# Kernel optimization log

Measured on AMD Instinct MI355X. Metric: run time of the kernel, lower is better.

## Reference

```python
import jax, jax.numpy as jnp
import numpy as np

N_NODES = 50000


def _gcn_conv(x, src, dst, W, b, n_nodes):
    # x: [N, Fin] -> h: [N, Fout]; GCN: D^-1/2 (A+I) D^-1/2 (x W) + b
    h = x @ W
    deg = jax.ops.segment_sum(jnp.ones_like(dst, dtype=h.dtype), dst,
                              num_segments=n_nodes)
    dinv = jax.lax.rsqrt(jnp.maximum(deg, 1.0))
    norm = dinv[src] * dinv[dst]                      # [E]
    msg = h[src] * norm[:, None]                      # [E, Fout] gather
    agg = jax.ops.segment_sum(msg, dst, num_segments=n_nodes)  # scatter-add
    return agg + b


def setup_inputs() -> dict:
    key = jax.random.key(0)
    k0, k1, k2, k3 = jax.random.split(key, 4)
    N, E, F_IN, H, C = N_NODES, 800000, 128, 128, 16
    x = jax.random.normal(k0, (N, F_IN), dtype=jnp.float32)
    edge_index = jax.random.randint(k1, (2, E), 0, N, dtype=jnp.int64)
    W1 = jax.random.normal(k2, (F_IN, H), dtype=jnp.float32) / np.sqrt(F_IN)
    b1 = jnp.zeros((H,), dtype=jnp.float32)
    W2 = jax.random.normal(k3, (H, C), dtype=jnp.float32) / np.sqrt(H)
    b2 = jnp.zeros((C,), dtype=jnp.float32)
    return {"x": x, "edge_index": edge_index, "W1": W1, "b1": b1,
            "W2": W2, "b2": b2}


def reference(x, edge_index, W1, b1, W2, b2):
    n = x.shape[0]
    # add self-loops (shared by both conv layers)
    loops = jnp.arange(n, dtype=edge_index.dtype)
    src = jnp.concatenate([edge_index[0], loops])
    dst = jnp.concatenate([edge_index[1], loops])
    h = _gcn_conv(x, src, dst, W1, b1, n)
    h = jax.nn.relu(h)
    # dropout p=0.5 is identity in eval mode
    h = _gcn_conv(h, src, dst, W2, b2, n)
    return jax.nn.log_softmax(h, axis=1)
```

## Files before the change

### kernel.cpp

```cpp
#include <hip/hip_runtime.h>
#include <hip/hip_fp16.h>
#include <math.h>


#define NBUCKET_SHIFT 8
#define BIN_CHUNK 4096
#define PAD_SLOP (7 << NBUCKET_SHIFT)
#define CAP  5120
#define CCAP (CAP + PAD_SLOP)

typedef __bf16 bf16x8 __attribute__((ext_vector_type(8)));
typedef float  f32x4  __attribute__((ext_vector_type(4)));
typedef float  f32x2  __attribute__((ext_vector_type(2)));

__device__ __forceinline__ unsigned short pack_bf16(float f) {
    unsigned u = __float_as_uint(f);
    return (unsigned short)((u + 0x7fffu + ((u >> 16) & 1u)) >> 16);
}

__device__ __forceinline__ void acc_fp8x16_fma(f32x2* a, uint4 v, float w) {
    f32x2 ww; ww.x = w; ww.y = w;
    a[0] += __builtin_amdgcn_cvt_pk_f32_fp8(v.x, false) * ww;
    a[1] += __builtin_amdgcn_cvt_pk_f32_fp8(v.x, true)  * ww;
    a[2] += __builtin_amdgcn_cvt_pk_f32_fp8(v.y, false) * ww;
    a[3] += __builtin_amdgcn_cvt_pk_f32_fp8(v.y, true)  * ww;
    a[4] += __builtin_amdgcn_cvt_pk_f32_fp8(v.z, false) * ww;
    a[5] += __builtin_amdgcn_cvt_pk_f32_fp8(v.z, true)  * ww;
    a[6] += __builtin_amdgcn_cvt_pk_f32_fp8(v.w, false) * ww;
    a[7] += __builtin_amdgcn_cvt_pk_f32_fp8(v.w, true)  * ww;
}

__device__ __forceinline__ void acc_fp16x8(f32x2* a, uint4 v) {
    float2 f;
    f = __half22float2(*(const __half2*)&v.x); a[0] += *(f32x2*)&f;
    f = __half22float2(*(const __half2*)&v.y); a[1] += *(f32x2*)&f;
    f = __half22float2(*(const __half2*)&v.z); a[2] += *(f32x2*)&f;
    f = __half22float2(*(const __half2*)&v.w); a[3] += *(f32x2*)&f;
}

union K1Smem {
    struct { unsigned spair[BIN_CHUNK]; int lcnt[256]; int lbase[256]; } b;
    unsigned short wtp[16384];
    float outb[4][16 * 132];
};

__global__ __launch_bounds__(256)
void bin_gemm1_kernel(const int* __restrict__ src, const int* __restrict__ dst,
                      int* __restrict__ bcur, unsigned* __restrict__ pairs,
                      int E, int nbuckets, int nbins,
                      const float* __restrict__ x, const float* __restrict__ W1,
                      unsigned* __restrict__ h1b, int N) {
    __shared__ K1Smem sm;
    const int blk = blockIdx.x;
    const int tid = threadIdx.x;

    if (blk < nbins) {
        const int e0 = blk * BIN_CHUNK;
        const int cnt = min(BIN_CHUNK, E - e0);
        sm.b.lcnt[tid] = 0;
        __syncthreads();
        for (int i = tid; i < cnt; i += 256) {
            unsigned s = (unsigned)src[e0 + i], d = (unsigned)dst[e0 + i];
            sm.b.spair[i] = (d >> NBUCKET_SHIFT) << 24 | (d & 255u) << 16 | s;
            atomicAdd(&sm.b.lcnt[d >> NBUCKET_SHIFT], 1);
        }
        __syncthreads();
        if (tid < nbuckets) {
            int c = sm.b.lcnt[tid];
            sm.b.lbase[tid] = (c > 0) ? atomicAdd(&bcur[tid], c) : 0;
            sm.b.lcnt[tid] = 0;
        }
        __syncthreads();
        for (int i = tid; i < cnt; i += 256) {
            unsigned p = sm.b.spair[i];
            int b = (int)(p >> 24);
            int off = atomicAdd(&sm.b.lcnt[b], 1);
            pairs[b * CAP + sm.b.lbase[b] + off] = p;
        }
        return;
    }

    const int gblk = blk - nbins;
    const int wave = tid >> 6, lane = tid & 63;
    const int q = lane >> 4, m = lane & 15;
    const int row0 = gblk * 64 + wave * 16;
    const int row = row0 + m;
    const int rowc = (row < N) ? row : (N - 1);

    for (int it = tid; it < 16384; it += 256) {
        int k = it >> 7, n = it & 127;
        int t = n >> 4, mm = n & 15;
        int ks = k >> 5;
        int lane2 = (((k & 31) >> 3) << 4) | mm;
        int j = k & 7;
        sm.wtp[(t * 4 + ks) * 512 + lane2 * 8 + j] = pack_bf16(W1[it]);
    }
    __syncthreads();

    f32x4 acc[8];
#pragma unroll
    for (int t = 0; t < 8; t++) acc[t] = (f32x4)0.0f;

#pragma unroll
    for (int ks = 0; ks < 4; ks++) {
        const float4* xp = (const float4*)(x + (size_t)rowc * 128 + ks * 32 + q * 8);
        float4 f0 = xp[0], f1 = xp[1];
        float fv[8] = {f0.x, f0.y, f0.z, f0.w, f1.x, f1.y, f1.z, f1.w};
        bf16x8 ah, al;
#pragma unroll
        for (int j = 0; j < 8; j++) {
            __bf16 h = (__bf16)fv[j];
            ah[j] = h;
            al[j] = (__bf16)(fv[j] - (float)h);
        }
#pragma unroll
        for (int t = 0; t < 8; t++) {
            bf16x8 b = *(const bf16x8*)(sm.wtp + (size_t)(t * 4 + ks) * 512 + lane * 8);
            acc[t] = __builtin_amdgcn_mfma_f32_16x16x32_bf16(ah, b, acc[t], 0, 0, 0);
            acc[t] = __builtin_amdgcn_mfma_f32_16x16x32_bf16(al, b, acc[t], 0, 0, 0);
        }
    }
    __syncthreads();

#pragma unroll
    for (int t = 0; t < 8; t++)
#pragma unroll
        for (int r = 0; r < 4; r++)
            sm.outb[wave][(q * 4 + r) * 132 + t * 16 + m] = acc[t][r];
    __syncthreads();

    const int r2 = lane >> 2, j = lane & 3;
    const int orow = row0 + r2;
    if (orow < N) {
        const float* lrow = &sm.outb[wave][r2 * 132];
#pragma unroll
        for (int s = 0; s < 4; s++) {
            float4 a = *(const float4*)(lrow + s * 32 + j * 8);
            float4 b = *(const float4*)(lrow + s * 32 + j * 8 + 4);
            unsigned lo = __builtin_amdgcn_cvt_pk_fp8_f32(a.x, a.y, 0, false);
            lo = __builtin_amdgcn_cvt_pk_fp8_f32(a.z, a.w, lo, true);
            unsigned hi = __builtin_amdgcn_cvt_pk_fp8_f32(b.x, b.y, 0, false);
            hi = __builtin_amdgcn_cvt_pk_fp8_f32(b.z, b.w, hi, true);
            ((uint2*)h1b)[(size_t)orow * 16 + s * 4 + j] = make_uint2(lo, hi);
        }
    }
}

__global__ __launch_bounds__(256)
void bucket_build_kernel(const int* __restrict__ bcur, const unsigned* __restrict__ pairs,
                         int* __restrict__ rowptr, int* __restrict__ rowcnt,
                         float* __restrict__ dinv, int* __restrict__ colsrc,
                         unsigned* __restrict__ h1b, unsigned* __restrict__ h2u,
                         int N, int nbuckets) {
    __shared__ int cnt[256];
    __shared__ int sm[256];
    const int tid = threadIdx.x;
    const int blk = blockIdx.x;
    const int nb0 = blk << NBUCKET_SHIFT;

    if (blk == 0) {
        if (tid < 32) h1b[(size_t)N * 32 + tid] = 0u;
        else if (tid < 40) h2u[(size_t)N * 8 + (tid - 32)] = 0u;
        else if (tid == 40) dinv[N] = 0.0f;
    }

    const int lo = blk * CAP;
    const int hi = lo + bcur[blk];
    cnt[tid] = 0;
    __syncthreads();

    for (int i = lo + tid; i < hi; i += 256)
        atomicAdd(&cnt[(int)(pairs[i] >> 16) & 255], 1);
    __syncthreads();

    int v = cnt[tid];
    int pdeg = (v + 7) & ~7;
    sm[tid] = pdeg;
    __syncthreads();
#pragma unroll
    for (int off = 1; off < 256; off <<= 1) {
        int u = (tid >= off) ? sm[tid - off] : 0;
        __syncthreads();
        sm[tid] += u;
        __syncthreads();
    }
    int pexcl = sm[tid] - pdeg;
    const int start = blk * CCAP + pexcl;
    int node = nb0 + tid;
    if (node < N) {
        rowptr[node] = start;
        rowcnt[node] = pdeg;
        dinv[node] = rsqrtf((float)v + 1.0f);
    }
    __syncthreads();
    cnt[tid] = start;
    __syncthreads();
    for (int i = lo + tid; i < hi; i += 256) {
        unsigned p = pairs[i];
        int pos = atomicAdd(&cnt[(int)(p >> 16) & 255], 1);
        colsrc[pos] = (int)(p & 0xffffu);
    }
    for (int p = start + v; p < start + pdeg; ++p)
        colsrc[p] = N;
}

__global__ __launch_bounds__(256)
void l1_fused_kernel(const int* __restrict__ rowptr, const int* __restrict__ rowcnt,
                     const int* __restrict__ colsrc,
                     const float* __restrict__ dinv, const unsigned* __restrict__ h1b,
                     const float* __restrict__ b1, const float* __restrict__ W2,
                     __half* __restrict__ h2s, int N) {
    __shared__ float rows[4][2][132];
    __shared__ float w2s[128 * 16];
    const int tid = threadIdx.x;
    const int wave = tid >> 6, lane = tid & 63;
    const int c = lane & 7;
    const int g = (lane >> 3) & 3;
    const int n = lane >> 5;
    const int d = blockIdx.x * 8 + wave * 2 + n;

    for (int i = tid; i < 512; i += 256)
        ((float4*)w2s)[i] = ((const float4*)W2)[i];

    const uint4* hq = (const uint4*)h1b;

    if (d < N) {
        const float dvd = dinv[d];
        f32x2 a[8];
#pragma unroll
        for (int j = 0; j < 8; j++) a[j] = (f32x2)0.0f;

        if (g == 0)
            acc_fp8x16_fma(a, hq[(size_t)d * 8 + c], dvd);

        int i = rowptr[d];
        const int end = i + rowcnt[d];
        int s0 = 0, s1 = 0, s2 = 0, s3 = 0;
        if (i + 16 <= end) {
            s0 = colsrc[i + g];      s1 = colsrc[i + g + 4];
            s2 = colsrc[i + g + 8];  s3 = colsrc[i + g + 12];
        }
        while (i + 16 <= end) {
            uint4 v0 = hq[(size_t)s0 * 8 + c];
            uint4 v1 = hq[(size_t)s1 * 8 + c];
            uint4 v2 = hq[(size_t)s2 * 8 + c];
            uint4 v3 = hq[(size_t)s3 * 8 + c];
            float w0 = dinv[s0], w1 = dinv[s1], w2 = dinv[s2], w3 = dinv[s3];
            i += 16;
            if (i + 16 <= end) {
                s0 = colsrc[i + g];      s1 = colsrc[i + g + 4];
                s2 = colsrc[i + g + 8];  s3 = colsrc[i + g + 12];
            }
            acc_fp8x16_fma(a, v0, w0); acc_fp8x16_fma(a, v1, w1);
            acc_fp8x16_fma(a, v2, w2); acc_fp8x16_fma(a, v3, w3);
        }
        for (; i + 4 <= end; i += 4) {
            int sx = colsrc[i + g];
            acc_fp8x16_fma(a, hq[(size_t)sx * 8 + c], dinv[sx]);
        }

#pragma unroll
        for (int j = 0; j < 8; j++) {
            a[j].x += __shfl_xor(a[j].x, 8, 64);
            a[j].y += __shfl_xor(a[j].y, 8, 64);
            a[j].x += __shfl_xor(a[j].x, 16, 64);
            a[j].y += __shfl_xor(a[j].y, 16, 64);
        }

        if (g == 0) {
            float* rbase = &rows[wave][n][c * 16];
#pragma unroll
            for (int t = 0; t < 4; t++) {
                float4 bb = ((const float4*)b1)[c * 4 + t];
                float4 o;
                o.x = fmaxf(a[2 * t].x * dvd + bb.x, 0.0f);
                o.y = fmaxf(a[2 * t].y * dvd + bb.y, 0.0f);
                o.z = fmaxf(a[2 * t + 1].x * dvd + bb.z, 0.0f);
                o.w = fmaxf(a[2 * t + 1].y * dvd + bb.w, 0.0f);
                *(float4*)(rbase + 4 * t) = o;
            }
        }
    }
    __syncthreads();

    const int n2 = lane >> 5, kh = (lane >> 4) & 1, col = lane & 15;
    const int d2 = blockIdx.x * 8 + wave * 2 + n2;
    if (d2 < N) {
        const float* r = &rows[wave][n2][kh * 64];
        const float* w = &w2s[kh * 64 * 16];
        float p = 0.0f;
#pragma unroll
        for (int k = 0; k < 64; k++)
            p = fmaf(r[k], w[k * 16 + col], p);
        p += __shfl_xor(p, 16, 64);
        if (kh == 0)
            h2s[(size_t)d2 * 16 + col] = __float2half_rn(p * dinv[d2]);
    }
}

__global__ __launch_bounds__(256)
void l2_kernel(const int* __restrict__ rowptr, const int* __restrict__ rowcnt,
               const int* __restrict__ colsrc,
               const float* __restrict__ dinv, const unsigned* __restrict__ h2s,
               const float* __restrict__ b2, float* __restrict__ out, int N) {
    const int tid = threadIdx.x;
    const int wave = tid >> 6, lane = tid & 63;
    const int n = lane >> 4;
    const int g = (lane >> 1) & 7;
    const int c = lane & 1;
    const int d = blockIdx.x * 16 + wave * 4 + n;
    if (d >= N) return;
    const uint4* h2q = (const uint4*)h2s;

    f32x2 a[4];
#pragma unroll
    for (int j = 0; j < 4; j++) a[j] = (f32x2)0.0f;

    if (g == 0)
        acc_fp16x8(a, h2q[(size_t)d * 2 + c]);

    int i = rowptr[d];
    const int end = i + rowcnt[d];
    uint4 v; int s2 = 0;
    if (i < end) {
        int s = colsrc[i + g];
        v = h2q[(size_t)s * 2 + c];
    }
    if (i + 8 < end) s2 = colsrc[i + 8 + g];
    while (i < end) {
        uint4 vc = v;
        if (i + 8 < end) v = h2q[(size_t)s2 * 2 + c];
        if (i + 16 < end) s2 = colsrc[i + 16 + g];
        i += 8;
        acc_fp16x8(a, vc);
    }

#pragma unroll
    for (int j = 0; j < 4; j++) {
#pragma unroll
        for (int off = 2; off <= 8; off <<= 1) {
            a[j].x += __shfl_xor(a[j].x, off, 64);
            a[j].y += __shfl_xor(a[j].y, off, 64);
        }
    }

    const float dv = dinv[d];
    const float* af = (const float*)a;
    float v8[8];
#pragma unroll
    for (int j = 0; j < 8; j++) v8[j] = af[j] * dv + b2[c * 8 + j];

    float m = v8[0];
#pragma unroll
    for (int j = 1; j < 8; j++) m = fmaxf(m, v8[j]);
    m = fmaxf(m, __shfl_xor(m, 1, 64));
    float e = 0.0f;
#pragma unroll
    for (int j = 0; j < 8; j++) e += expf(v8[j] - m);
    e += __shfl_xor(e, 1, 64);
    float lse = m + logf(e);

    if (g == 0) {
        float4 o0 = make_float4(v8[0] - lse, v8[1] - lse, v8[2] - lse, v8[3] - lse);
        float4 o1 = make_float4(v8[4] - lse, v8[5] - lse, v8[6] - lse, v8[7] - lse);
        float4* op = (float4*)(out + (size_t)d * 16 + c * 8);
        op[0] = o0; op[1] = o1;
    }
}

extern "C" void kernel_launch(void* const* d_in, const int* in_sizes, int n_in,
                              void* d_out, int out_size, void* d_ws, size_t ws_size,
                              hipStream_t stream) {
    const float* x  = (const float*)d_in[0];
    const int*  ei  = (const int*)d_in[1];
    const float* W1 = (const float*)d_in[2];
    const float* b1 = (const float*)d_in[3];
    const float* W2 = (const float*)d_in[4];
    const float* b2 = (const float*)d_in[5];
    float* out = (float*)d_out;

    const int N = in_sizes[0] / 128;
    const int E = in_sizes[1] / 2;
    const int* src = ei;
    const int* dst = ei + E;
    const int nbuckets = (N + 255) >> NBUCKET_SHIFT;
    const int nbins = (E + BIN_CHUNK - 1) / BIN_CHUNK;
    const int g1blocks = (N + 63) / 64;

    float*          wsf     = (float*)d_ws;
    float*          dinv    = wsf;
    int*            rowptr  = (int*)(wsf + N + 16);
    int*            rowcnt  = rowptr + N;
    int*            bcur    = rowcnt + N;
    int*            colsrc  = bcur + 256;
    unsigned*       pairs   = (unsigned*)(colsrc + (size_t)nbuckets * CCAP);
    unsigned*       h1b     = pairs + (size_t)nbuckets * CAP;
    unsigned*       h2u     = h1b + (size_t)(N + 1) * 32;

    hipMemsetAsync(bcur, 0, 256 * sizeof(int), stream);
    bin_gemm1_kernel<<<nbins + g1blocks, 256, 0, stream>>>(src, dst, bcur, pairs,
                                                           E, nbuckets, nbins,
                                                           x, W1, h1b, N);

    bucket_build_kernel<<<nbuckets, 256, 0, stream>>>(bcur, pairs, rowptr, rowcnt,
                                                      dinv, colsrc, h1b, h2u,
                                                      N, nbuckets);

    l1_fused_kernel<<<(N + 7) / 8, 256, 0, stream>>>(rowptr, rowcnt, colsrc, dinv,
                                                     h1b, b1, W2, (__half*)h2u, N);

    l2_kernel<<<(N + 15) / 16, 256, 0, stream>>>(rowptr, rowcnt, colsrc, dinv, h2u,
                                                 b2, out, N);
}
```

Baseline: 160.3 us.

## Split layer-1 features into two 64-column halves and accumulate partial GEMM2 atomically

Stores the fp8 hidden features as two separate 64-column planes, so the layer-1 gather kernel processes one half per block and the per-neighbour gather footprint per plane is halved, which should improve cache locality. Each half computes a partial product with its slice of W2 and atomically adds into an fp32 h2 accumulator that is zeroed by an enlarged memset. Layer 2 now gathers fp32 rows and folds the source-side dinv scaling into the gather instead of the stored fp16 pre-scaled values. The cost is twice as many gather passes over colsrc and dinv, extra atomics, a larger memset, and doubled bytes per layer-2 gather.

```diff
diff --git a/kernel.cpp b/kernel.cpp
--- a/kernel.cpp
+++ b/kernel.cpp
@@ -30,14 +30,6 @@
     a[7] += __builtin_amdgcn_cvt_pk_f32_fp8(v.w, true)  * ww;
 }
 
-__device__ __forceinline__ void acc_fp16x8(f32x2* a, uint4 v) {
-    float2 f;
-    f = __half22float2(*(const __half2*)&v.x); a[0] += *(f32x2*)&f;
-    f = __half22float2(*(const __half2*)&v.y); a[1] += *(f32x2*)&f;
-    f = __half22float2(*(const __half2*)&v.z); a[2] += *(f32x2*)&f;
-    f = __half22float2(*(const __half2*)&v.w); a[3] += *(f32x2*)&f;
-}
-
 union K1Smem {
     struct { unsigned spair[BIN_CHUNK]; int lcnt[256]; int lbase[256]; } b;
     unsigned short wtp[16384];
@@ -141,7 +133,8 @@
             lo = __builtin_amdgcn_cvt_pk_fp8_f32(a.z, a.w, lo, true);
             unsigned hi = __builtin_amdgcn_cvt_pk_fp8_f32(b.x, b.y, 0, false);
             hi = __builtin_amdgcn_cvt_pk_fp8_f32(b.z, b.w, hi, true);
-            ((uint2*)h1b)[(size_t)orow * 16 + s * 4 + j] = make_uint2(lo, hi);
+            ((uint2*)h1b)[((size_t)(s >> 1) * (N + 1) + orow) * 8 + (s & 1) * 4 + j]
+                = make_uint2(lo, hi);
         }
     }
 }
@@ -150,8 +143,7 @@
 void bucket_build_kernel(const int* __restrict__ bcur, const unsigned* __restrict__ pairs,
                          int* __restrict__ rowptr, int* __restrict__ rowcnt,
                          float* __restrict__ dinv, int* __restrict__ colsrc,
-                         unsigned* __restrict__ h1b, unsigned* __restrict__ h2u,
-                         int N, int nbuckets) {
+                         unsigned* __restrict__ h1b, int N, int nbuckets) {
     __shared__ int cnt[256];
     __shared__ int sm[256];
     const int tid = threadIdx.x;
@@ -159,9 +151,9 @@
     const int nb0 = blk << NBUCKET_SHIFT;
 
     if (blk == 0) {
-        if (tid < 32) h1b[(size_t)N * 32 + tid] = 0u;
-        else if (tid < 40) h2u[(size_t)N * 8 + (tid - 32)] = 0u;
-        else if (tid == 40) dinv[N] = 0.0f;
+        if (tid < 16) h1b[((size_t)0 * (N + 1) + N) * 16 + tid] = 0u;
+        else if (tid < 32) h1b[((size_t)1 * (N + 1) + N) * 16 + (tid - 16)] = 0u;
+        else if (tid == 32) dinv[N] = 0.0f;
     }
 
     const int lo = blk * CAP;
@@ -209,20 +201,21 @@
                      const int* __restrict__ colsrc,
                      const float* __restrict__ dinv, const unsigned* __restrict__ h1b,
                      const float* __restrict__ b1, const float* __restrict__ W2,
-                     __half* __restrict__ h2s, int N) {
-    __shared__ float rows[4][2][132];
-    __shared__ float w2s[128 * 16];
+                     float* __restrict__ h2acc, int N) {
+    __shared__ float rows[4][4][68];
+    __shared__ float w2s[64 * 16];
     const int tid = threadIdx.x;
     const int wave = tid >> 6, lane = tid & 63;
-    const int c = lane & 7;
-    const int g = (lane >> 3) & 3;
-    const int n = lane >> 5;
-    const int d = blockIdx.x * 8 + wave * 2 + n;
-
-    for (int i = tid; i < 512; i += 256)
-        ((float4*)w2s)[i] = ((const float4*)W2)[i];
-
-    const uint4* hq = (const uint4*)h1b;
+    const int c = lane & 3;
+    const int g = (lane >> 2) & 3;
+    const int n = lane >> 4;
+    const int p = blockIdx.x & 1;
+    const int d = (blockIdx.x >> 1) * 16 + wave * 4 + n;
+
+    for (int i = tid; i < 256; i += 256)
+        ((float4*)w2s)[i] = ((const float4*)W2)[p * 256 + i];
+
+    const uint4* hq = (const uint4*)h1b + (size_t)p * (N + 1) * 4;
 
     if (d < N) {
         const float dvd = dinv[d];
@@ -231,7 +224,7 @@
         for (int j = 0; j < 8; j++) a[j] = (f32x2)0.0f;
 
         if (g == 0)
-            acc_fp8x16_fma(a, hq[(size_t)d * 8 + c], dvd);
+            acc_fp8x16_fma(a, hq[(size_t)d * 4 + c], dvd);
 
         int i = rowptr[d];
         const int end = i + rowcnt[d];
@@ -241,10 +234,10 @@
             s2 = colsrc[i + g + 8];  s3 = colsrc[i + g + 12];
         }
         while (i + 16 <= end) {
-            uint4 v0 = hq[(size_t)s0 * 8 + c];
-            uint4 v1 = hq[(size_t)s1 * 8 + c];
-            uint4 v2 = hq[(size_t)s2 * 8 + c];
-            uint4 v3 = hq[(size_t)s3 * 8 + c];
+            uint4 v0 = hq[(size_t)s0 * 4 + c];
+            uint4 v1 = hq[(size_t)s1 * 4 + c];
+            uint4 v2 = hq[(size_t)s2 * 4 + c];
+            uint4 v3 = hq[(size_t)s3 * 4 + c];
             float w0 = dinv[s0], w1 = dinv[s1], w2 = dinv[s2], w3 = dinv[s3];
             i += 16;
             if (i + 16 <= end) {
@@ -256,22 +249,22 @@
         }
         for (; i + 4 <= end; i += 4) {
             int sx = colsrc[i + g];
-            acc_fp8x16_fma(a, hq[(size_t)sx * 8 + c], dinv[sx]);
+            acc_fp8x16_fma(a, hq[(size_t)sx * 4 + c], dinv[sx]);
         }
 
 #pragma unroll
         for (int j = 0; j < 8; j++) {
+            a[j].x += __shfl_xor(a[j].x, 4, 64);
+            a[j].y += __shfl_xor(a[j].y, 4, 64);
             a[j].x += __shfl_xor(a[j].x, 8, 64);
             a[j].y += __shfl_xor(a[j].y, 8, 64);
-            a[j].x += __shfl_xor(a[j].x, 16, 64);
-            a[j].y += __shfl_xor(a[j].y, 16, 64);
         }
 
         if (g == 0) {
             float* rbase = &rows[wave][n][c * 16];
 #pragma unroll
             for (int t = 0; t < 4; t++) {
-                float4 bb = ((const float4*)b1)[c * 4 + t];
+                float4 bb = ((const float4*)b1)[p * 16 + c * 4 + t];
                 float4 o;
                 o.x = fmaxf(a[2 * t].x * dvd + bb.x, 0.0f);
                 o.y = fmaxf(a[2 * t].y * dvd + bb.y, 0.0f);
@@ -283,89 +276,94 @@
     }
     __syncthreads();
 
-    const int n2 = lane >> 5, kh = (lane >> 4) & 1, col = lane & 15;
-    const int d2 = blockIdx.x * 8 + wave * 2 + n2;
+    const int n2 = lane >> 4, col = lane & 15;
+    const int d2 = (blockIdx.x >> 1) * 16 + wave * 4 + n2;
     if (d2 < N) {
-        const float* r = &rows[wave][n2][kh * 64];
-        const float* w = &w2s[kh * 64 * 16];
-        float p = 0.0f;
-#pragma unroll
-        for (int k = 0; k < 64; k++)
-            p = fmaf(r[k], w[k * 16 + col], p);
-        p += __shfl_xor(p, 16, 64);
-        if (kh == 0)
-            h2s[(size_t)d2 * 16 + col] = __float2half_rn(p * dinv[d2]);
+        const float* r = &rows[wave][n2][0];
+        float p0 = 0.0f, p1 = 0.0f;
+#pragma unroll
+        for (int k = 0; k < 32; k++) {
+            p0 = fmaf(r[k],      w2s[k * 16 + col],        p0);
+            p1 = fmaf(r[k + 32], w2s[(k + 32) * 16 + col], p1);
+        }
+        atomicAdd(&h2acc[(size_t)d2 * 16 + col], p0 + p1);
     }
 }
 
 __global__ __launch_bounds__(256)
 void l2_kernel(const int* __restrict__ rowptr, const int* __restrict__ rowcnt,
                const int* __restrict__ colsrc,
-               const float* __restrict__ dinv, const unsigned* __restrict__ h2s,
+               const float* __restrict__ dinv, const float* __restrict__ h2acc,
                const float* __restrict__ b2, float* __restrict__ out, int N) {
     const int tid = threadIdx.x;
     const int wave = tid >> 6, lane = tid & 63;
     const int n = lane >> 4;
-    const int g = (lane >> 1) & 7;
-    const int c = lane & 1;
+    const int g = (lane >> 2) & 3;
+    const int c = lane & 3;
     const int d = blockIdx.x * 16 + wave * 4 + n;
     if (d >= N) return;
-    const uint4* h2q = (const uint4*)h2s;
-
-    f32x2 a[4];
-#pragma unroll
-    for (int j = 0; j < 4; j++) a[j] = (f32x2)0.0f;
-
-    if (g == 0)
-        acc_fp16x8(a, h2q[(size_t)d * 2 + c]);
+    const float4* zq = (const float4*)h2acc;
+
+    float ax = 0.f, ay = 0.f, az = 0.f, aw = 0.f;
+    const float dv = dinv[d];
+    if (g == 0) {
+        float4 z = zq[(size_t)d * 4 + c];
+        ax = z.x * dv; ay = z.y * dv; az = z.z * dv; aw = z.w * dv;
+    }
 
     int i = rowptr[d];
     const int end = i + rowcnt[d];
-    uint4 v; int s2 = 0;
-    if (i < end) {
-        int s = colsrc[i + g];
-        v = h2q[(size_t)s * 2 + c];
-    }
-    if (i + 8 < end) s2 = colsrc[i + 8 + g];
-    while (i < end) {
-        uint4 vc = v;
-        if (i + 8 < end) v = h2q[(size_t)s2 * 2 + c];
-        if (i + 16 < end) s2 = colsrc[i + 16 + g];
-        i += 8;
-        acc_fp16x8(a, vc);
-    }
-
-#pragma unroll
-    for (int j = 0; j < 4; j++) {
-#pragma unroll
-        for (int off = 2; off <= 8; off <<= 1) {
-            a[j].x += __shfl_xor(a[j].x, off, 64);
-            a[j].y += __shfl_xor(a[j].y, off, 64);
-        }
-    }
-
-    const float dv = dinv[d];
-    const float* af = (const float*)a;
-    float v8[8];
-#pragma unroll
-    for (int j = 0; j < 8; j++) v8[j] = af[j] * dv + b2[c * 8 + j];
-
-    float m = v8[0];
-#pragma unroll
-    for (int j = 1; j < 8; j++) m = fmaxf(m, v8[j]);
+    int s0 = 0, s1 = 0, s2 = 0, s3 = 0;
+    if (i + 16 <= end) {
+        s0 = colsrc[i + g];      s1 = colsrc[i + g + 4];
+        s2 = colsrc[i + g + 8];  s3 = colsrc[i + g + 12];
+    }
+    while (i + 16 <= end) {
+        float4 v0 = zq[(size_t)s0 * 4 + c];
+        float4 v1 = zq[(size_t)s1 * 4 + c];
+        float4 v2 = zq[(size_t)s2 * 4 + c];
+        float4 v3 = zq[(size_t)s3 * 4 + c];
+        float w0 = dinv[s0], w1 = dinv[s1], w2 = dinv[s2], w3 = dinv[s3];
+        i += 16;
+        if (i + 16 <= end) {
+            s0 = colsrc[i + g];      s1 = colsrc[i + g + 4];
+            s2 = colsrc[i + g + 8];  s3 = colsrc[i + g + 12];
+        }
+        ax = fmaf(v0.x, w0, ax); ay = fmaf(v0.y, w0, ay);
+        az = fmaf(v0.z, w0, az); aw = fmaf(v0.w, w0, aw);
+        ax = fmaf(v1.x, w1, ax); ay = fmaf(v1.y, w1, ay);
+        az = fmaf(v1.z, w1, az); aw = fmaf(v1.w, w1, aw);
+        ax = fmaf(v2.x, w2, ax); ay = fmaf(v2.y, w2, ay);
+        az = fmaf(v2.z, w2, az); aw = fmaf(v2.w, w2, aw);
+        ax = fmaf(v3.x, w3, ax); ay = fmaf(v3.y, w3, ay);
+        az = fmaf(v3.z, w3, az); aw = fmaf(v3.w, w3, aw);
+    }
+    for (; i + 4 <= end; i += 4) {
+        int sx = colsrc[i + g];
+        float4 v = zq[(size_t)sx * 4 + c];
+        float w = dinv[sx];
+        ax = fmaf(v.x, w, ax); ay = fmaf(v.y, w, ay);
+        az = fmaf(v.z, w, az); aw = fmaf(v.w, w, aw);
+    }
+
+    ax += __shfl_xor(ax, 4, 64); ay += __shfl_xor(ay, 4, 64);
+    az += __shfl_xor(az, 4, 64); aw += __shfl_xor(aw, 4, 64);
+    ax += __shfl_xor(ax, 8, 64); ay += __shfl_xor(ay, 8, 64);
+    az += __shfl_xor(az, 8, 64); aw += __shfl_xor(aw, 8, 64);
+
+    float4 b = ((const float4*)b2)[c];
+    float4 val = make_float4(ax * dv + b.x, ay * dv + b.y,
+                             az * dv + b.z, aw * dv + b.w);
+    float m = fmaxf(fmaxf(val.x, val.y), fmaxf(val.z, val.w));
     m = fmaxf(m, __shfl_xor(m, 1, 64));
-    float e = 0.0f;
-#pragma unroll
-    for (int j = 0; j < 8; j++) e += expf(v8[j] - m);
+    m = fmaxf(m, __shfl_xor(m, 2, 64));
+    float e = expf(val.x - m) + expf(val.y - m) + expf(val.z - m) + expf(val.w - m);
     e += __shfl_xor(e, 1, 64);
+    e += __shfl_xor(e, 2, 64);
     float lse = m + logf(e);
-
-    if (g == 0) {
-        float4 o0 = make_float4(v8[0] - lse, v8[1] - lse, v8[2] - lse, v8[3] - lse);
-        float4 o1 = make_float4(v8[4] - lse, v8[5] - lse, v8[6] - lse, v8[7] - lse);
-        float4* op = (float4*)(out + (size_t)d * 16 + c * 8);
-        op[0] = o0; op[1] = o1;
-    }
+    if (g == 0)
+        ((float4*)out)[(size_t)d * 4 + c] =
+            make_float4(val.x - lse, val.y - lse, val.z - lse, val.w - lse);
 }
 
 extern "C" void kernel_launch(void* const* d_in, const int* in_sizes, int n_in,
@@ -392,23 +390,23 @@
     int*            rowptr  = (int*)(wsf + N + 16);
     int*            rowcnt  = rowptr + N;
     int*            bcur    = rowcnt + N;
-    int*            colsrc  = bcur + 256;
+    float*          h2acc   = (float*)(bcur + 256);
+    int*            colsrc  = (int*)(h2acc + (size_t)(N + 1) * 16);
     unsigned*       pairs   = (unsigned*)(colsrc + (size_t)nbuckets * CCAP);
     unsigned*       h1b     = pairs + (size_t)nbuckets * CAP;
-    unsigned*       h2u     = h1b + (size_t)(N + 1) * 32;
-
-    hipMemsetAsync(bcur, 0, 256 * sizeof(int), stream);
+
+    hipMemsetAsync(bcur, 0, (256 + (size_t)(N + 1) * 16) * sizeof(int), stream);
     bin_gemm1_kernel<<<nbins + g1blocks, 256, 0, stream>>>(src, dst, bcur, pairs,
                                                            E, nbuckets, nbins,
                                                            x, W1, h1b, N);
 
     bucket_build_kernel<<<nbuckets, 256, 0, stream>>>(bcur, pairs, rowptr, rowcnt,
-                                                      dinv, colsrc, h1b, h2u,
-                                                      N, nbuckets);
-
-    l1_fused_kernel<<<(N + 7) / 8, 256, 0, stream>>>(rowptr, rowcnt, colsrc, dinv,
-                                                     h1b, b1, W2, (__half*)h2u, N);
-
-    l2_kernel<<<(N + 15) / 16, 256, 0, stream>>>(rowptr, rowcnt, colsrc, dinv, h2u,
-                                                 b2, out, N);
-}
+                                                      dinv, colsrc, h1b, N, nbuckets);
+
+    l1_fused_kernel<<<((N + 15) / 16) * 2, 256, 0, stream>>>(rowptr, rowcnt, colsrc,
+                                                             dinv, h1b, b1, W2,
+                                                             h2acc, N);
+
+    l2_kernel<<<(N + 15) / 16, 256, 0, stream>>>(rowptr, rowcnt, colsrc, dinv,
+                                                 h2acc, b2, out, N);
+}
```

Result: no change. 158.9 us (-0.8%).

## Split layer-1 aggregation into two feature halves with atomic layer-2 projection

Applied to the files above, without the earlier changes.

The fp8 h1 table is stored as two column-halves of 64 features each, and the layer-1 gather kernel now runs two blocks per node group, each gathering only one half, so each pass's working set is smaller and more likely to stay in cache. Each half computes a partial 64x16 product with W2 and atomically adds it into an fp32 buffer that is zeroed in the same memset. A new small kernel scales that buffer by dinv and converts it to fp16 for layer 2. Separately, the hi/lo bf16 split in GEMM1 is dropped, which halves the MFMA count at some cost in precision. The change adds an extra launch, atomic traffic and a larger memset, and gathers colsrc twice.

```diff
diff --git a/kernel.cpp b/kernel.cpp
--- a/kernel.cpp
+++ b/kernel.cpp
@@ -106,18 +106,13 @@
         const float4* xp = (const float4*)(x + (size_t)rowc * 128 + ks * 32 + q * 8);
         float4 f0 = xp[0], f1 = xp[1];
         float fv[8] = {f0.x, f0.y, f0.z, f0.w, f1.x, f1.y, f1.z, f1.w};
-        bf16x8 ah, al;
-#pragma unroll
-        for (int j = 0; j < 8; j++) {
-            __bf16 h = (__bf16)fv[j];
-            ah[j] = h;
-            al[j] = (__bf16)(fv[j] - (float)h);
-        }
+        bf16x8 ah;
+#pragma unroll
+        for (int j = 0; j < 8; j++) ah[j] = (__bf16)fv[j];
 #pragma unroll
         for (int t = 0; t < 8; t++) {
             bf16x8 b = *(const bf16x8*)(sm.wtp + (size_t)(t * 4 + ks) * 512 + lane * 8);
             acc[t] = __builtin_amdgcn_mfma_f32_16x16x32_bf16(ah, b, acc[t], 0, 0, 0);
-            acc[t] = __builtin_amdgcn_mfma_f32_16x16x32_bf16(al, b, acc[t], 0, 0, 0);
         }
     }
     __syncthreads();
@@ -141,7 +136,8 @@
             lo = __builtin_amdgcn_cvt_pk_fp8_f32(a.z, a.w, lo, true);
             unsigned hi = __builtin_amdgcn_cvt_pk_fp8_f32(b.x, b.y, 0, false);
             hi = __builtin_amdgcn_cvt_pk_fp8_f32(b.z, b.w, hi, true);
-            ((uint2*)h1b)[(size_t)orow * 16 + s * 4 + j] = make_uint2(lo, hi);
+            ((uint2*)h1b)[((size_t)(s >> 1) * (N + 1) + orow) * 8 + (s & 1) * 4 + j]
+                = make_uint2(lo, hi);
         }
     }
 }
@@ -150,8 +146,7 @@
 void bucket_build_kernel(const int* __restrict__ bcur, const unsigned* __restrict__ pairs,
                          int* __restrict__ rowptr, int* __restrict__ rowcnt,
                          float* __restrict__ dinv, int* __restrict__ colsrc,
-                         unsigned* __restrict__ h1b, unsigned* __restrict__ h2u,
-                         int N, int nbuckets) {
+                         unsigned* __restrict__ h1b, int N, int nbuckets) {
     __shared__ int cnt[256];
     __shared__ int sm[256];
     const int tid = threadIdx.x;
@@ -159,9 +154,9 @@
     const int nb0 = blk << NBUCKET_SHIFT;
 
     if (blk == 0) {
-        if (tid < 32) h1b[(size_t)N * 32 + tid] = 0u;
-        else if (tid < 40) h2u[(size_t)N * 8 + (tid - 32)] = 0u;
-        else if (tid == 40) dinv[N] = 0.0f;
+        if (tid < 16) h1b[((size_t)0 * (N + 1) + N) * 16 + tid] = 0u;
+        else if (tid < 32) h1b[((size_t)1 * (N + 1) + N) * 16 + (tid - 16)] = 0u;
+        else if (tid == 32) dinv[N] = 0.0f;
     }
 
     const int lo = blk * CAP;
@@ -209,20 +204,21 @@
                      const int* __restrict__ colsrc,
                      const float* __restrict__ dinv, const unsigned* __restrict__ h1b,
                      const float* __restrict__ b1, const float* __restrict__ W2,
-                     __half* __restrict__ h2s, int N) {
-    __shared__ float rows[4][2][132];
-    __shared__ float w2s[128 * 16];
+                     float* __restrict__ h2acc, int N) {
+    __shared__ float rows[4][4][68];
+    __shared__ float w2s[64 * 16];
     const int tid = threadIdx.x;
     const int wave = tid >> 6, lane = tid & 63;
-    const int c = lane & 7;
-    const int g = (lane >> 3) & 3;
-    const int n = lane >> 5;
-    const int d = blockIdx.x * 8 + wave * 2 + n;
-
-    for (int i = tid; i < 512; i += 256)
-        ((float4*)w2s)[i] = ((const float4*)W2)[i];
-
-    const uint4* hq = (const uint4*)h1b;
+    const int c = lane & 3;
+    const int g = (lane >> 2) & 3;
+    const int n = lane >> 4;
+    const int p = blockIdx.x & 1;
+    const int d = (blockIdx.x >> 1) * 16 + wave * 4 + n;
+
+    for (int i = tid; i < 256; i += 256)
+        ((float4*)w2s)[i] = ((const float4*)W2)[p * 256 + i];
+
+    const uint4* hq = (const uint4*)h1b + (size_t)p * (N + 1) * 4;
 
     if (d < N) {
         const float dvd = dinv[d];
@@ -231,7 +227,7 @@
         for (int j = 0; j < 8; j++) a[j] = (f32x2)0.0f;
 
         if (g == 0)
-            acc_fp8x16_fma(a, hq[(size_t)d * 8 + c], dvd);
+            acc_fp8x16_fma(a, hq[(size_t)d * 4 + c], dvd);
 
         int i = rowptr[d];
         const int end = i + rowcnt[d];
@@ -241,10 +237,10 @@
             s2 = colsrc[i + g + 8];  s3 = colsrc[i + g + 12];
         }
         while (i + 16 <= end) {
-            uint4 v0 = hq[(size_t)s0 * 8 + c];
-            uint4 v1 = hq[(size_t)s1 * 8 + c];
-            uint4 v2 = hq[(size_t)s2 * 8 + c];
-            uint4 v3 = hq[(size_t)s3 * 8 + c];
+            uint4 v0 = hq[(size_t)s0 * 4 + c];
+            uint4 v1 = hq[(size_t)s1 * 4 + c];
+            uint4 v2 = hq[(size_t)s2 * 4 + c];
+            uint4 v3 = hq[(size_t)s3 * 4 + c];
             float w0 = dinv[s0], w1 = dinv[s1], w2 = dinv[s2], w3 = dinv[s3];
             i += 16;
             if (i + 16 <= end) {
@@ -256,22 +252,22 @@
         }
         for (; i + 4 <= end; i += 4) {
             int sx = colsrc[i + g];
-            acc_fp8x16_fma(a, hq[(size_t)sx * 8 + c], dinv[sx]);
+            acc_fp8x16_fma(a, hq[(size_t)sx * 4 + c], dinv[sx]);
         }
 
 #pragma unroll
         for (int j = 0; j < 8; j++) {
+            a[j].x += __shfl_xor(a[j].x, 4, 64);
+            a[j].y += __shfl_xor(a[j].y, 4, 64);
             a[j].x += __shfl_xor(a[j].x, 8, 64);
             a[j].y += __shfl_xor(a[j].y, 8, 64);
-            a[j].x += __shfl_xor(a[j].x, 16, 64);
-            a[j].y += __shfl_xor(a[j].y, 16, 64);
         }
 
         if (g == 0) {
             float* rbase = &rows[wave][n][c * 16];
 #pragma unroll
             for (int t = 0; t < 4; t++) {
-                float4 bb = ((const float4*)b1)[c * 4 + t];
+                float4 bb = ((const float4*)b1)[p * 16 + c * 4 + t];
                 float4 o;
                 o.x = fmaxf(a[2 * t].x * dvd + bb.x, 0.0f);
                 o.y = fmaxf(a[2 * t].y * dvd + bb.y, 0.0f);
@@ -283,19 +279,30 @@
     }
     __syncthreads();
 
-    const int n2 = lane >> 5, kh = (lane >> 4) & 1, col = lane & 15;
-    const int d2 = blockIdx.x * 8 + wave * 2 + n2;
+    const int n2 = lane >> 4, col = lane & 15;
+    const int d2 = (blockIdx.x >> 1) * 16 + wave * 4 + n2;
     if (d2 < N) {
-        const float* r = &rows[wave][n2][kh * 64];
-        const float* w = &w2s[kh * 64 * 16];
-        float p = 0.0f;
-#pragma unroll
-        for (int k = 0; k < 64; k++)
-            p = fmaf(r[k], w[k * 16 + col], p);
-        p += __shfl_xor(p, 16, 64);
-        if (kh == 0)
-            h2s[(size_t)d2 * 16 + col] = __float2half_rn(p * dinv[d2]);
-    }
+        const float* r = &rows[wave][n2][0];
+        float p0 = 0.0f, p1 = 0.0f;
+#pragma unroll
+        for (int k = 0; k < 32; k++) {
+            p0 = fmaf(r[k],      w2s[k * 16 + col],        p0);
+            p1 = fmaf(r[k + 32], w2s[(k + 32) * 16 + col], p1);
+        }
+        atomicAdd(&h2acc[(size_t)d2 * 16 + col], p0 + p1);
+    }
+}
+
+__global__ __launch_bounds__(256)
+void h2cvt_kernel(const float* __restrict__ h2acc, const float* __restrict__ dinv,
+                  unsigned* __restrict__ h2h, int N) {
+    int idx = blockIdx.x * 256 + threadIdx.x;
+    if (idx >= (N + 1) * 4) return;
+    float dv = dinv[idx >> 2];
+    float4 v = ((const float4*)h2acc)[idx];
+    __half2 lo = __floats2half2_rn(v.x * dv, v.y * dv);
+    __half2 hi = __floats2half2_rn(v.z * dv, v.w * dv);
+    ((uint2*)h2h)[idx] = make_uint2(*(unsigned*)&lo, *(unsigned*)&hi);
 }
 
 __global__ __launch_bounds__(256)
@@ -392,23 +399,26 @@
     int*            rowptr  = (int*)(wsf + N + 16);
     int*            rowcnt  = rowptr + N;
     int*            bcur    = rowcnt + N;
-    int*            colsrc  = bcur + 256;
+    float*          h2acc   = (float*)(bcur + 256);
+    int*            colsrc  = (int*)(h2acc + (size_t)(N + 1) * 16);
     unsigned*       pairs   = (unsigned*)(colsrc + (size_t)nbuckets * CCAP);
     unsigned*       h1b     = pairs + (size_t)nbuckets * CAP;
-    unsigned*       h2u     = h1b + (size_t)(N + 1) * 32;
-
-    hipMemsetAsync(bcur, 0, 256 * sizeof(int), stream);
+    unsigned*       h2h     = pairs;
+
+    hipMemsetAsync(bcur, 0, (256 + (size_t)(N + 1) * 16) * sizeof(int), stream);
     bin_gemm1_kernel<<<nbins + g1blocks, 256, 0, stream>>>(src, dst, bcur, pairs,
                                                            E, nbuckets, nbins,
                                                            x, W1, h1b, N);
 
     bucket_build_kernel<<<nbuckets, 256, 0, stream>>>(bcur, pairs, rowptr, rowcnt,
-                                                      dinv, colsrc, h1b, h2u,
-                                                      N, nbuckets);
-
-    l1_fused_kernel<<<(N + 7) / 8, 256, 0, stream>>>(rowptr, rowcnt, colsrc, dinv,
-                                                     h1b, b1, W2, (__half*)h2u, N);
-
-    l2_kernel<<<(N + 15) / 16, 256, 0, stream>>>(rowptr, rowcnt, colsrc, dinv, h2u,
+                                                      dinv, colsrc, h1b, N, nbuckets);
+
+    l1_fused_kernel<<<((N + 15) / 16) * 2, 256, 0, stream>>>(rowptr, rowcnt, colsrc,
+                                                             dinv, h1b, b1, W2,
+                                                             h2acc, N);
+
+    h2cvt_kernel<<<((N + 1) * 4 + 255) / 256, 256, 0, stream>>>(h2acc, dinv, h2h, N);
+
+    l2_kernel<<<(N + 15) / 16, 256, 0, stream>>>(rowptr, rowcnt, colsrc, dinv, h2h,
                                                  b2, out, N);
 }
```

Measured after the change: 158.4 us (median of 2 runs). Within noise of the previous version (-1.2%).
